# Kernel tuning notes

Measured on AMD Instinct MI355X. Metric: run time of the kernel, lower is better.

The kernel has to match this reference:

```python
import jax, jax.numpy as jnp
import numpy as np

N_NODES = 100000
N_EDGES = 800000
IN_CH = 100
HID = 100   # 2 * out_channels
OUT = 50


def setup_inputs() -> dict:
    key = jax.random.key(0)
    ks = jax.random.split(key, 6)
    x = jax.random.normal(ks[0], (N_NODES, IN_CH), dtype=jnp.float32)
    edge_index = jax.random.randint(ks[1], (2, N_EDGES), 0, N_NODES, dtype=jnp.int32)
    # Glorot-ish init for the three GCN layer weights; zero biases.
    W1 = jax.random.normal(ks[2], (IN_CH, HID), dtype=jnp.float32) * (1.0 / np.sqrt(IN_CH))
    b1 = jnp.zeros((HID,), dtype=jnp.float32)
    W_mu = jax.random.normal(ks[3], (HID, OUT), dtype=jnp.float32) * (1.0 / np.sqrt(HID))
    b_mu = jnp.zeros((OUT,), dtype=jnp.float32)
    W_ls = jax.random.normal(ks[4], (HID, OUT), dtype=jnp.float32) * (1.0 / np.sqrt(HID))
    b_ls = jnp.zeros((OUT,), dtype=jnp.float32)
    return {"x": x, "edge_index": edge_index, "W1": W1, "b1": b1,
            "W_mu": W_mu, "b_mu": b_mu, "W_ls": W_ls, "b_ls": b_ls}


def _gcn_conv(x, W, b, src, dst, deg_inv_sqrt, n):
    # GCNConv: out = D^-1/2 (A + I) D^-1/2 (x W) + b
    h = x @ W                                      # transform first (smaller messages)
    norm = deg_inv_sqrt[src] * deg_inv_sqrt[dst]   # [E]
    agg = jax.ops.segment_sum(h[src] * norm[:, None], dst, num_segments=n)
    agg = agg + h * (deg_inv_sqrt * deg_inv_sqrt)[:, None]  # self-loop term
    return agg + b


def reference(x, edge_index, W1, b1, W_mu, b_mu, W_ls, b_ls):
    n = x.shape[0]
    src, dst = edge_index[0], edge_index[1]
    # degree with self-loops (GCN normalization, edge_weight = 1)
    deg = jax.ops.segment_sum(jnp.ones((edge_index.shape[1],), jnp.float32), dst,
                              num_segments=n) + 1.0
    deg_inv_sqrt = jax.lax.rsqrt(deg)
    h = jax.nn.relu(_gcn_conv(x, W1, b1, src, dst, deg_inv_sqrt, n))
    # dropout is identity in eval mode (p applied only during training)
    mu = _gcn_conv(h, W_mu, b_mu, src, dst, deg_inv_sqrt, n)
    logstd = _gcn_conv(h, W_ls, b_ls, src, dst, deg_inv_sqrt, n)
    return mu, logstd
```

## Files before the change

### kernel.cpp

```cpp
#include <hip/hip_runtime.h>

#define NN 100000
#define NE 800000
#define NBLK 196
#define BCAP 6144
#define EPB 8192
#define NPART ((NE + EPB - 1) / EPB)
#define PACKBLK 56

typedef unsigned short ushort_t;
typedef unsigned int uint_t;
typedef __attribute__((ext_vector_type(8))) short short8;
typedef __attribute__((ext_vector_type(4))) float floatx4;

__device__ __forceinline__ float bf2f(ushort_t u) {
    union { unsigned int i; float f; } v; v.i = ((unsigned int)u) << 16; return v.f;
}
__device__ __forceinline__ ushort_t f2bf(float f) {
    union { float f; unsigned int i; } v; v.f = f;
    unsigned int b = v.i + 0x7FFF + ((v.i >> 16) & 1);
    return (ushort_t)(b >> 16);
}
__device__ __forceinline__ uint_t pack2(float a, float b) {
    return (uint_t)f2bf(a) | ((uint_t)f2bf(b) << 16);
}

__global__ __launch_bounds__(256) void k_part(const int* __restrict__ src,
                                              const int* __restrict__ dst,
                                              int* __restrict__ bcnt,
                                              int* __restrict__ bedge,
                                              const float* __restrict__ W1,
                                              const float* __restrict__ Wmu,
                                              const float* __restrict__ Wls,
                                              uint_t* __restrict__ Wt1g,
                                              uint_t* __restrict__ Wt2g) {
    __shared__ int hist[NBLK];
    __shared__ int lbase[NBLK];
    const int blk = blockIdx.x, t = threadIdx.x;

    if (blk >= NPART) {
        int lidx = (blk - NPART) * 256 + t;
        int np = lidx >> 6;
        int kp = lidx & 63;
        int mat = np / 112, n = np - mat * 112;
        int k0 = kp * 2, k1 = k0 + 1;
        float w0 = 0.0f, w1 = 0.0f;
        if (mat == 0) {
            if (n < 100) {
                if (k0 < 100) w0 = W1[k0 * 100 + n];
                if (k1 < 100) w1 = W1[k1 * 100 + n];
            }
            Wt1g[n * 64 + kp] = pack2(w0, w1);
        } else {
            if (n < 50) {
                if (k0 < 100) w0 = Wmu[k0 * 50 + n];
                if (k1 < 100) w1 = Wmu[k1 * 50 + n];
            } else if (n < 100) {
                if (k0 < 100) w0 = Wls[k0 * 50 + (n - 50)];
                if (k1 < 100) w1 = Wls[k1 * 50 + (n - 50)];
            }
            Wt2g[n * 64 + kp] = pack2(w0, w1);
        }
        return;
    }

    const int e0 = blk * EPB;
    const int e1 = (e0 + EPB < NE) ? e0 + EPB : NE;

    if (t < NBLK) hist[t] = 0;
    __syncthreads();
    for (int e = e0 + t; e < e1; e += 256)
        atomicAdd(&hist[dst[e] >> 9], 1);
    __syncthreads();
    if (t < NBLK) {
        int h = hist[t];
        lbase[t] = (h > 0) ? atomicAdd(&bcnt[t], h) : 0;
    }
    __syncthreads();
    if (t < NBLK) hist[t] = lbase[t];
    __syncthreads();
    for (int e = e0 + t; e < e1; e += 256) {
        int d = dst[e];
        int b = d >> 9;
        int pos = atomicAdd(&hist[b], 1);
        bedge[b * BCAP + pos] = src[e] | ((d & 511) << 17);
    }
}

__global__ __launch_bounds__(256) void k_build(const int* __restrict__ bcnt,
                                               const int* __restrict__ bedge,
                                               float* __restrict__ dis,
                                               int* __restrict__ off,
                                               int* __restrict__ ssrc) {
    __shared__ int eb[BCAP];
    __shared__ int hist[512];
    __shared__ int sc[2][512];
    __shared__ int red[4];
    const int b = blockIdx.x, t = threadIdx.x;
    const int cnt = bcnt[b];
    const int* be = bedge + (size_t)b * BCAP;
    const int g0 = b * 512;

    hist[t] = 0; hist[t + 256] = 0;
    int part = (t < b) ? bcnt[t] : 0;
    #pragma unroll
    for (int o = 32; o > 0; o >>= 1) part += __shfl_down(part, o, 64);
    if ((t & 63) == 0) red[t >> 6] = part;
    __syncthreads();

    for (int i = t; i < cnt; i += 256) {
        int v = be[i];
        eb[i] = v;
        atomicAdd(&hist[v >> 17], 1);
    }
    __syncthreads();
    const int base0 = red[0] + red[1] + red[2] + red[3];

    sc[0][t] = hist[t];
    sc[0][t + 256] = hist[t + 256];
    __syncthreads();
    int c = 0;
    for (int o = 1; o < 512; o <<= 1) {
        int nxt = c ^ 1;
        #pragma unroll
        for (int q = 0; q < 2; ++q) {
            int j = t + q * 256;
            sc[nxt][j] = sc[c][j] + ((j >= o) ? sc[c][j - o] : 0);
        }
        c = nxt;
        __syncthreads();
    }

    #pragma unroll
    for (int q = 0; q < 2; ++q) {
        int j = t + q * 256, g = g0 + j;
        int o = base0 + ((j > 0) ? sc[c][j - 1] : 0);
        if (g < NN) dis[g] = rsqrtf((float)hist[j] + 1.0f);
        if (g <= NN) off[g] = o;
        hist[j] = o;
    }
    __syncthreads();

    for (int i = t; i < cnt; i += 256) {
        int v = eb[i];
        int pos = atomicAdd(&hist[v >> 17], 1);
        ssrc[pos] = v & 0x1FFFF;
    }
}

__global__ __launch_bounds__(256) void k_gemm1_mfma(
    const float* __restrict__ X, const uint_t* __restrict__ Wtg,
    const float* __restrict__ dis,
    ushort_t* __restrict__ H)
{
    __shared__ ushort_t Ws[112 * 136];
    const int tid = threadIdx.x;
    const int row0 = blockIdx.x * 64;

    for (int idx = tid; idx < 112 * 16; idx += 256) {
        int n = idx >> 4, c = idx & 15;
        uint4 v = *(const uint4*)&Wtg[n * 64 + c * 4];
        *(uint4*)&Ws[n * 136 + c * 8] = v;
    }
    __syncthreads();

    const int wave = tid >> 6, lane = tid & 63;
    const int quad = lane >> 4, l16 = lane & 15;
    int row = row0 + wave * 16 + l16;
    if (row >= NN) row = NN - 1;
    const float* xp = X + (size_t)row * 100;

    floatx4 acc[7];
    #pragma unroll
    for (int t = 0; t < 7; ++t) acc[t] = (floatx4){0.f, 0.f, 0.f, 0.f};

    #pragma unroll
    for (int ks = 0; ks < 4; ++ks) {
        const int kb = ks * 32 + quad * 8;
        short8 af;
        if (ks < 3) {
            float4 u = *(const float4*)&xp[kb];
            float4 v = *(const float4*)&xp[kb + 4];
            af[0] = (short)f2bf(u.x); af[1] = (short)f2bf(u.y);
            af[2] = (short)f2bf(u.z); af[3] = (short)f2bf(u.w);
            af[4] = (short)f2bf(v.x); af[5] = (short)f2bf(v.y);
            af[6] = (short)f2bf(v.z); af[7] = (short)f2bf(v.w);
        } else {
            af = (short8){0, 0, 0, 0, 0, 0, 0, 0};
            if (quad == 0) {
                float4 u = *(const float4*)&xp[96];
                af[0] = (short)f2bf(u.x); af[1] = (short)f2bf(u.y);
                af[2] = (short)f2bf(u.z); af[3] = (short)f2bf(u.w);
            }
        }
        #pragma unroll
        for (int t = 0; t < 7; ++t) {
            short8 bf = *(const short8*)&Ws[(t * 16 + l16) * 136 + kb];
            acc[t] = __builtin_amdgcn_mfma_f32_16x16x32_bf16(af, bf, acc[t], 0, 0, 0);
        }
    }

    const int mbase = row0 + wave * 16 + quad * 4;
    #pragma unroll
    for (int reg = 0; reg < 4; ++reg) {
        int m = mbase + reg;
        if (m >= NN) continue;
        float dd = dis[m];
        #pragma unroll
        for (int t = 0; t < 7; ++t) {
            int n = t * 16 + l16;
            H[(size_t)m * 128 + n] = (n < 100) ? f2bf(acc[t][reg] * dd) : (ushort_t)0;
        }
        H[(size_t)m * 128 + 112 + l16] = 0;
    }
}

__global__ __launch_bounds__(256) void k_gemm2_mfma(
    const ushort_t* __restrict__ A,
    const uint_t* __restrict__ Wtg,
    const float* __restrict__ bmu, const float* __restrict__ bls,
    float* __restrict__ outmu, float* __restrict__ outls)
{
    __shared__ ushort_t Ws[112 * 136];
    const int tid = threadIdx.x;
    const int row0 = blockIdx.x * 64;

    for (int idx = tid; idx < 112 * 16; idx += 256) {
        int n = idx >> 4, c = idx & 15;
        uint4 v = *(const uint4*)&Wtg[n * 64 + c * 4];
        *(uint4*)&Ws[n * 136 + c * 8] = v;
    }
    __syncthreads();

    const int wave = tid >> 6, lane = tid & 63;
    const int quad = lane >> 4, l16 = lane & 15;
    int arow = row0 + wave * 16 + l16;
    if (arow >= NN) arow = NN - 1;

    floatx4 acc[7];
    #pragma unroll
    for (int t = 0; t < 7; ++t) acc[t] = (floatx4){0.f, 0.f, 0.f, 0.f};

    #pragma unroll
    for (int k0 = 0; k0 < 128; k0 += 32) {
        short8 af = *(const short8*)&A[(size_t)arow * 128 + k0 + quad * 8];
        #pragma unroll
        for (int t = 0; t < 7; ++t) {
            short8 bf = *(const short8*)&Ws[(t * 16 + l16) * 136 + k0 + quad * 8];
            acc[t] = __builtin_amdgcn_mfma_f32_16x16x32_bf16(af, bf, acc[t], 0, 0, 0);
        }
    }

    const int mbase = row0 + wave * 16 + quad * 4;
    #pragma unroll
    for (int reg = 0; reg < 4; ++reg) {
        int m = mbase + reg;
        if (m >= NN) continue;
        #pragma unroll
        for (int t = 0; t < 7; ++t) {
            int n = t * 16 + l16;
            if (n < 50) {
                outmu[(size_t)m * 50 + n] = acc[t][reg] + bmu[n];
            } else if (n < 100) {
                outls[(size_t)m * 50 + (n - 50)] = acc[t][reg] + bls[n - 50];
            }
        }
    }
}

template<int PHASE>
__global__ __launch_bounds__(256) void k_agg(
    const ushort_t* __restrict__ Hin,
    const int* __restrict__ off, const int* __restrict__ ssrc,
    const float* __restrict__ dis, const float* __restrict__ bias,
    ushort_t* __restrict__ outb)
{
    int i = blockIdx.x * 256 + threadIdx.x;
    if (i >= NN * 8) return;
    int node = i >> 3;
    int col = (i & 7) * 16;

    float a[16];
    {
        short8 u = *(const short8*)(Hin + (size_t)node * 128 + col);
        short8 v = *(const short8*)(Hin + (size_t)node * 128 + col + 8);
        #pragma unroll
        for (int j = 0; j < 8; ++j) { a[j] = bf2f((ushort_t)u[j]); a[8 + j] = bf2f((ushort_t)v[j]); }
    }

    int e0 = off[node], e1 = off[node + 1];
    int e = e0;
    for (; e + 3 < e1; e += 4) {
        int s0 = ssrc[e], s1 = ssrc[e + 1], s2 = ssrc[e + 2], s3 = ssrc[e + 3];
        short8 u0 = *(const short8*)(Hin + (size_t)s0 * 128 + col);
        short8 v0 = *(const short8*)(Hin + (size_t)s0 * 128 + col + 8);
        short8 u1 = *(const short8*)(Hin + (size_t)s1 * 128 + col);
        short8 v1 = *(const short8*)(Hin + (size_t)s1 * 128 + col + 8);
        short8 u2 = *(const short8*)(Hin + (size_t)s2 * 128 + col);
        short8 v2 = *(const short8*)(Hin + (size_t)s2 * 128 + col + 8);
        short8 u3 = *(const short8*)(Hin + (size_t)s3 * 128 + col);
        short8 v3 = *(const short8*)(Hin + (size_t)s3 * 128 + col + 8);
        #pragma unroll
        for (int j = 0; j < 8; ++j) {
            a[j]     += bf2f((ushort_t)u0[j]) + bf2f((ushort_t)u1[j])
                      + bf2f((ushort_t)u2[j]) + bf2f((ushort_t)u3[j]);
            a[8 + j] += bf2f((ushort_t)v0[j]) + bf2f((ushort_t)v1[j])
                      + bf2f((ushort_t)v2[j]) + bf2f((ushort_t)v3[j]);
        }
    }
    for (; e < e1; ++e) {
        int s0 = ssrc[e];
        short8 u0 = *(const short8*)(Hin + (size_t)s0 * 128 + col);
        short8 v0 = *(const short8*)(Hin + (size_t)s0 * 128 + col + 8);
        #pragma unroll
        for (int j = 0; j < 8; ++j) {
            a[j] += bf2f((ushort_t)u0[j]);
            a[8 + j] += bf2f((ushort_t)v0[j]);
        }
    }

    float d = dis[node];
    short8 o0, o1;
    if (PHASE == 1) {
        float b[16];
        #pragma unroll
        for (int j = 0; j < 16; ++j) {
            int cj = col + j;
            b[j] = (cj < 100) ? bias[cj] : 0.0f;
        }
        #pragma unroll
        for (int j = 0; j < 8; ++j) {
            float h0 = fmaxf(a[j] * d + b[j], 0.0f) * d;
            float h1 = fmaxf(a[8 + j] * d + b[8 + j], 0.0f) * d;
            o0[j] = (short)f2bf(h0);
            o1[j] = (short)f2bf(h1);
        }
    } else {
        #pragma unroll
        for (int j = 0; j < 8; ++j) {
            o0[j] = (short)f2bf(a[j] * d);
            o1[j] = (short)f2bf(a[8 + j] * d);
        }
    }
    *(short8*)(outb + (size_t)node * 128 + col) = o0;
    *(short8*)(outb + (size_t)node * 128 + col + 8) = o1;
}

extern "C" void kernel_launch(void* const* d_in, const int* in_sizes, int n_in,
                              void* d_out, int out_size, void* d_ws, size_t ws_size,
                              hipStream_t stream)
{
    const float* x   = (const float*)d_in[0];
    const int*   ei  = (const int*)d_in[1];
    const float* W1  = (const float*)d_in[2];
    const float* b1  = (const float*)d_in[3];
    const float* Wmu = (const float*)d_in[4];
    const float* bmu = (const float*)d_in[5];
    const float* Wls = (const float*)d_in[6];
    const float* bls = (const float*)d_in[7];
    float* out = (float*)d_out;

    const int* src = ei;
    const int* dst = ei + NE;

    int*   wsI  = (int*)d_ws;
    float* wsF  = (float*)d_ws;
    int*      off  = wsI + 100000;
    float*    dis  = wsF + 200704;
    uint_t*   Wt1g = (uint_t*)(wsI + 300704);
    uint_t*   Wt2g = (uint_t*)(wsI + 307872);
    int*      bcnt = wsI + 315040;
    int*      ssrc = wsI + 315296;
    int*      bedge= wsI + 1115296;
    ushort_t* H1b  = (ushort_t*)(wsI + 2319520);
    ushort_t* hb   = (ushort_t*)(wsI + 8719520);
    ushort_t* A2b  = (ushort_t*)(wsI + 15119520);

    hipMemsetAsync(bcnt, 0, 256 * sizeof(int), stream);
    k_part<<<NPART + PACKBLK, 256, 0, stream>>>(src, dst, bcnt, bedge,
                                                W1, Wmu, Wls, Wt1g, Wt2g);
    k_build<<<NBLK, 256, 0, stream>>>(bcnt, bedge, dis, off, ssrc);

    const int gblk = (NN + 63) / 64;
    k_gemm1_mfma<<<gblk, 256, 0, stream>>>(x, Wt1g, dis, H1b);
    k_agg<1><<<(NN * 8 + 255) / 256, 256, 0, stream>>>(H1b, off, ssrc, dis, b1, hb);
    k_agg<2><<<(NN * 8 + 255) / 256, 256, 0, stream>>>(hb, off, ssrc, dis, b1, A2b);
    k_gemm2_mfma<<<gblk, 256, 0, stream>>>(A2b, Wt2g, bmu, bls,
                                           out, out + (size_t)NN * 50);
}
```

Measured before the change: 247.2 us.

## Fuse second aggregation with output GEMM and widen build/partition parallelism

The second-layer neighbor aggregation now writes its normalized bf16 rows into shared memory, and the same block runs the MFMA GEMM for mu/logstd. This removes the A2b global round trip and one kernel launch. The build kernel now uses 512 threads with one histogram bin per thread, and the partition kernel uses smaller edge chunks to get more blocks. The trade-off is that the fused kernel loads the weight tile per 32-row block, and only two of its four waves run the MFMA stage.

```diff
diff --git a/kernel.cpp b/kernel.cpp
--- a/kernel.cpp
+++ b/kernel.cpp
@@ -4,7 +4,7 @@
 #define NE 800000
 #define NBLK 196
 #define BCAP 6144
-#define EPB 8192
+#define EPB 2048
 #define NPART ((NE + EPB - 1) / EPB)
 #define PACKBLK 56
 
@@ -87,7 +87,7 @@
     }
 }
 
-__global__ __launch_bounds__(256) void k_build(const int* __restrict__ bcnt,
+__global__ __launch_bounds__(512) void k_build(const int* __restrict__ bcnt,
                                                const int* __restrict__ bedge,
                                                float* __restrict__ dis,
                                                int* __restrict__ off,
@@ -95,53 +95,49 @@
     __shared__ int eb[BCAP];
     __shared__ int hist[512];
     __shared__ int sc[2][512];
-    __shared__ int red[4];
+    __shared__ int red[8];
     const int b = blockIdx.x, t = threadIdx.x;
     const int cnt = bcnt[b];
     const int* be = bedge + (size_t)b * BCAP;
     const int g0 = b * 512;
 
-    hist[t] = 0; hist[t + 256] = 0;
+    hist[t] = 0;
     int part = (t < b) ? bcnt[t] : 0;
     #pragma unroll
     for (int o = 32; o > 0; o >>= 1) part += __shfl_down(part, o, 64);
     if ((t & 63) == 0) red[t >> 6] = part;
     __syncthreads();
 
-    for (int i = t; i < cnt; i += 256) {
+    for (int i = t; i < cnt; i += 512) {
         int v = be[i];
         eb[i] = v;
         atomicAdd(&hist[v >> 17], 1);
     }
     __syncthreads();
-    const int base0 = red[0] + red[1] + red[2] + red[3];
+    int base0 = 0;
+    #pragma unroll
+    for (int r = 0; r < 8; ++r) base0 += red[r];
 
     sc[0][t] = hist[t];
-    sc[0][t + 256] = hist[t + 256];
     __syncthreads();
     int c = 0;
     for (int o = 1; o < 512; o <<= 1) {
         int nxt = c ^ 1;
-        #pragma unroll
-        for (int q = 0; q < 2; ++q) {
-            int j = t + q * 256;
-            sc[nxt][j] = sc[c][j] + ((j >= o) ? sc[c][j - o] : 0);
-        }
+        sc[nxt][t] = sc[c][t] + ((t >= o) ? sc[c][t - o] : 0);
         c = nxt;
         __syncthreads();
     }
 
-    #pragma unroll
-    for (int q = 0; q < 2; ++q) {
-        int j = t + q * 256, g = g0 + j;
-        int o = base0 + ((j > 0) ? sc[c][j - 1] : 0);
-        if (g < NN) dis[g] = rsqrtf((float)hist[j] + 1.0f);
-        if (g <= NN) off[g] = o;
-        hist[j] = o;
-    }
-    __syncthreads();
-
-    for (int i = t; i < cnt; i += 256) {
+    {
+        int g = g0 + t;
+        int ov = base0 + ((t > 0) ? sc[c][t - 1] : 0);
+        if (g < NN) dis[g] = rsqrtf((float)hist[t] + 1.0f);
+        if (g <= NN) off[g] = ov;
+        hist[t] = ov;
+    }
+    __syncthreads();
+
+    for (int i = t; i < cnt; i += 512) {
         int v = eb[i];
         int pos = atomicAdd(&hist[v >> 17], 1);
         ssrc[pos] = v & 0x1FFFF;
@@ -215,61 +211,7 @@
     }
 }
 
-__global__ __launch_bounds__(256) void k_gemm2_mfma(
-    const ushort_t* __restrict__ A,
-    const uint_t* __restrict__ Wtg,
-    const float* __restrict__ bmu, const float* __restrict__ bls,
-    float* __restrict__ outmu, float* __restrict__ outls)
-{
-    __shared__ ushort_t Ws[112 * 136];
-    const int tid = threadIdx.x;
-    const int row0 = blockIdx.x * 64;
-
-    for (int idx = tid; idx < 112 * 16; idx += 256) {
-        int n = idx >> 4, c = idx & 15;
-        uint4 v = *(const uint4*)&Wtg[n * 64 + c * 4];
-        *(uint4*)&Ws[n * 136 + c * 8] = v;
-    }
-    __syncthreads();
-
-    const int wave = tid >> 6, lane = tid & 63;
-    const int quad = lane >> 4, l16 = lane & 15;
-    int arow = row0 + wave * 16 + l16;
-    if (arow >= NN) arow = NN - 1;
-
-    floatx4 acc[7];
-    #pragma unroll
-    for (int t = 0; t < 7; ++t) acc[t] = (floatx4){0.f, 0.f, 0.f, 0.f};
-
-    #pragma unroll
-    for (int k0 = 0; k0 < 128; k0 += 32) {
-        short8 af = *(const short8*)&A[(size_t)arow * 128 + k0 + quad * 8];
-        #pragma unroll
-        for (int t = 0; t < 7; ++t) {
-            short8 bf = *(const short8*)&Ws[(t * 16 + l16) * 136 + k0 + quad * 8];
-            acc[t] = __builtin_amdgcn_mfma_f32_16x16x32_bf16(af, bf, acc[t], 0, 0, 0);
-        }
-    }
-
-    const int mbase = row0 + wave * 16 + quad * 4;
-    #pragma unroll
-    for (int reg = 0; reg < 4; ++reg) {
-        int m = mbase + reg;
-        if (m >= NN) continue;
-        #pragma unroll
-        for (int t = 0; t < 7; ++t) {
-            int n = t * 16 + l16;
-            if (n < 50) {
-                outmu[(size_t)m * 50 + n] = acc[t][reg] + bmu[n];
-            } else if (n < 100) {
-                outls[(size_t)m * 50 + (n - 50)] = acc[t][reg] + bls[n - 50];
-            }
-        }
-    }
-}
-
-template<int PHASE>
-__global__ __launch_bounds__(256) void k_agg(
+__global__ __launch_bounds__(256) void k_agg1(
     const ushort_t* __restrict__ Hin,
     const int* __restrict__ off, const int* __restrict__ ssrc,
     const float* __restrict__ dis, const float* __restrict__ bias,
@@ -321,29 +263,134 @@
 
     float d = dis[node];
     short8 o0, o1;
-    if (PHASE == 1) {
-        float b[16];
-        #pragma unroll
-        for (int j = 0; j < 16; ++j) {
-            int cj = col + j;
-            b[j] = (cj < 100) ? bias[cj] : 0.0f;
-        }
-        #pragma unroll
-        for (int j = 0; j < 8; ++j) {
-            float h0 = fmaxf(a[j] * d + b[j], 0.0f) * d;
-            float h1 = fmaxf(a[8 + j] * d + b[8 + j], 0.0f) * d;
-            o0[j] = (short)f2bf(h0);
-            o1[j] = (short)f2bf(h1);
-        }
-    } else {
+    float b[16];
+    #pragma unroll
+    for (int j = 0; j < 16; ++j) {
+        int cj = col + j;
+        b[j] = (cj < 100) ? bias[cj] : 0.0f;
+    }
+    #pragma unroll
+    for (int j = 0; j < 8; ++j) {
+        float h0 = fmaxf(a[j] * d + b[j], 0.0f) * d;
+        float h1 = fmaxf(a[8 + j] * d + b[8 + j], 0.0f) * d;
+        o0[j] = (short)f2bf(h0);
+        o1[j] = (short)f2bf(h1);
+    }
+    *(short8*)(outb + (size_t)node * 128 + col) = o0;
+    *(short8*)(outb + (size_t)node * 128 + col + 8) = o1;
+}
+
+__global__ __launch_bounds__(256) void k_fuse2(
+    const ushort_t* __restrict__ Hin,
+    const int* __restrict__ off, const int* __restrict__ ssrc,
+    const float* __restrict__ dis,
+    const uint_t* __restrict__ Wtg,
+    const float* __restrict__ bmu, const float* __restrict__ bls,
+    float* __restrict__ outmu, float* __restrict__ outls)
+{
+    __shared__ ushort_t Ws[112 * 136];
+    __shared__ ushort_t As[32][136];
+    const int tid = threadIdx.x;
+    const int row0 = blockIdx.x * 32;
+
+    for (int idx = tid; idx < 112 * 16; idx += 256) {
+        int n = idx >> 4, c = idx & 15;
+        uint4 v = *(const uint4*)&Wtg[n * 64 + c * 4];
+        *(uint4*)&Ws[n * 136 + c * 8] = v;
+    }
+
+    {
+        const int lr = tid >> 3;
+        const int col = (tid & 7) * 16;
+        int nd = row0 + lr;
+        if (nd >= NN) nd = NN - 1;
+
+        float a[16];
+        {
+            short8 u = *(const short8*)(Hin + (size_t)nd * 128 + col);
+            short8 v = *(const short8*)(Hin + (size_t)nd * 128 + col + 8);
+            #pragma unroll
+            for (int j = 0; j < 8; ++j) { a[j] = bf2f((ushort_t)u[j]); a[8 + j] = bf2f((ushort_t)v[j]); }
+        }
+
+        int e0 = off[nd], e1 = off[nd + 1];
+        int e = e0;
+        for (; e + 3 < e1; e += 4) {
+            int s0 = ssrc[e], s1 = ssrc[e + 1], s2 = ssrc[e + 2], s3 = ssrc[e + 3];
+            short8 u0 = *(const short8*)(Hin + (size_t)s0 * 128 + col);
+            short8 v0 = *(const short8*)(Hin + (size_t)s0 * 128 + col + 8);
+            short8 u1 = *(const short8*)(Hin + (size_t)s1 * 128 + col);
+            short8 v1 = *(const short8*)(Hin + (size_t)s1 * 128 + col + 8);
+            short8 u2 = *(const short8*)(Hin + (size_t)s2 * 128 + col);
+            short8 v2 = *(const short8*)(Hin + (size_t)s2 * 128 + col + 8);
+            short8 u3 = *(const short8*)(Hin + (size_t)s3 * 128 + col);
+            short8 v3 = *(const short8*)(Hin + (size_t)s3 * 128 + col + 8);
+            #pragma unroll
+            for (int j = 0; j < 8; ++j) {
+                a[j]     += bf2f((ushort_t)u0[j]) + bf2f((ushort_t)u1[j])
+                          + bf2f((ushort_t)u2[j]) + bf2f((ushort_t)u3[j]);
+                a[8 + j] += bf2f((ushort_t)v0[j]) + bf2f((ushort_t)v1[j])
+                          + bf2f((ushort_t)v2[j]) + bf2f((ushort_t)v3[j]);
+            }
+        }
+        for (; e < e1; ++e) {
+            int s0 = ssrc[e];
+            short8 u0 = *(const short8*)(Hin + (size_t)s0 * 128 + col);
+            short8 v0 = *(const short8*)(Hin + (size_t)s0 * 128 + col + 8);
+            #pragma unroll
+            for (int j = 0; j < 8; ++j) {
+                a[j] += bf2f((ushort_t)u0[j]);
+                a[8 + j] += bf2f((ushort_t)v0[j]);
+            }
+        }
+
+        const float d = dis[nd];
+        short8 o0, o1;
         #pragma unroll
         for (int j = 0; j < 8; ++j) {
             o0[j] = (short)f2bf(a[j] * d);
             o1[j] = (short)f2bf(a[8 + j] * d);
         }
-    }
-    *(short8*)(outb + (size_t)node * 128 + col) = o0;
-    *(short8*)(outb + (size_t)node * 128 + col + 8) = o1;
+        *(short8*)&As[lr][col] = o0;
+        *(short8*)&As[lr][col + 8] = o1;
+    }
+    __syncthreads();
+
+    const int wave = tid >> 6, lane = tid & 63;
+    if (wave < 2) {
+        const int quad = lane >> 4, l16 = lane & 15;
+        const int lrow = wave * 16 + l16;
+
+        floatx4 acc[7];
+        #pragma unroll
+        for (int t = 0; t < 7; ++t) acc[t] = (floatx4){0.f, 0.f, 0.f, 0.f};
+
+        #pragma unroll
+        for (int k0 = 0; k0 < 128; k0 += 32) {
+            short8 af = *(const short8*)&As[lrow][k0 + quad * 8];
+            #pragma unroll
+            for (int t = 0; t < 7; ++t) {
+                short8 bf = *(const short8*)&Ws[(t * 16 + l16) * 136 + k0 + quad * 8];
+                acc[t] = __builtin_amdgcn_mfma_f32_16x16x32_bf16(af, bf, acc[t], 0, 0, 0);
+            }
+        }
+
+        const int mbase = row0 + wave * 16 + quad * 4;
+        #pragma unroll
+        for (int reg = 0; reg < 4; ++reg) {
+            int m = mbase + reg;
+            if (m >= NN) continue;
+            #pragma unroll
+            for (int t = 0; t < 7; ++t) {
+                int n = t * 16 + l16;
+                if (n < 50) {
+                    outmu[(size_t)m * 50 + n] = acc[t][reg] + bmu[n];
+                } else if (n < 100) {
+                    outls[(size_t)m * 50 + (n - 50)] = acc[t][reg] + bls[n - 50];
+                }
+            }
+        }
+    }
 }
 
 extern "C" void kernel_launch(void* const* d_in, const int* in_sizes, int n_in,
@@ -374,17 +421,18 @@
     int*      bedge= wsI + 1115296;
     ushort_t* H1b  = (ushort_t*)(wsI + 2319520);
     ushort_t* hb   = (ushort_t*)(wsI + 8719520);
-    ushort_t* A2b  = (ushort_t*)(wsI + 15119520);
+    (void)ws_size;
 
     hipMemsetAsync(bcnt, 0, 256 * sizeof(int), stream);
     k_part<<<NPART + PACKBLK, 256, 0, stream>>>(src, dst, bcnt, bedge,
                                                 W1, Wmu, Wls, Wt1g, Wt2g);
-    k_build<<<NBLK, 256, 0, stream>>>(bcnt, bedge, dis, off, ssrc);
+    k_build<<<NBLK, 512, 0, stream>>>(bcnt, bedge, dis, off, ssrc);
 
     const int gblk = (NN + 63) / 64;
+    const int ablk = (NN * 8 + 255) / 256;
+    const int fblk = (NN + 31) / 32;
     k_gemm1_mfma<<<gblk, 256, 0, stream>>>(x, Wt1g, dis, H1b);
-    k_agg<1><<<(NN * 8 + 255) / 256, 256, 0, stream>>>(H1b, off, ssrc, dis, b1, hb);
-    k_agg<2><<<(NN * 8 + 255) / 256, 256, 0, stream>>>(hb, off, ssrc, dis, b1, A2b);
-    k_gemm2_mfma<<<gblk, 256, 0, stream>>>(A2b, Wt2g, bmu, bls,
-                                           out, out + (size_t)NN * 50);
-}
+    k_agg1<<<ablk, 256, 0, stream>>>(H1b, off, ssrc, dis, b1, hb);
+    k_fuse2<<<fblk, 256, 0, stream>>>(hb, off, ssrc, dis, Wt2g, bmu, bls,
+                                      out, out + (size_t)NN * 50);
+}
```

Result: faster. 233.3 us (-5.6%).
